# Optimization experiments

Hardware: AMD Instinct MI355X
Metric: run time of the kernel (lower is better)

Reference implementation:

```python
import jax, jax.numpy as jnp
import numpy as np

B, T, D = 2, 2048, 1024
H = 16
HD = D // H
NE = 17  # n_edge_types + 1

def setup_inputs() -> dict:
    key = jax.random.key(0)
    ks = jax.random.split(key, 6)
    x = jax.random.normal(ks[0], (B, T, D), dtype=jnp.float32)
    graph_adj = jax.random.uniform(ks[1], (B, T, T), dtype=jnp.float32)
    edge_types = jax.random.randint(ks[2], (B, T, T), 0, NE, dtype=jnp.int32)
    Wqkv = jax.random.normal(ks[3], (D, 3 * D), dtype=jnp.float32) * (D ** -0.5)
    Wproj = jax.random.normal(ks[4], (D, D), dtype=jnp.float32) * (D ** -0.5)
    adj_bias = jnp.zeros((H,), dtype=jnp.float32)
    edge_table = jax.random.normal(ks[5], (NE, H), dtype=jnp.float32) * 0.02
    return {"x": x, "graph_adj": graph_adj, "edge_types": edge_types,
            "Wqkv": Wqkv, "Wproj": Wproj, "adj_bias": adj_bias,
            "edge_table": edge_table}

def reference(x, graph_adj, edge_types, Wqkv, Wproj, adj_bias, edge_table):
    Bc, Tc, C = x.shape
    qkv = (x @ Wqkv).reshape(Bc, Tc, 3, H, HD)
    q, k, v = qkv[:, :, 0], qkv[:, :, 1], qkv[:, :, 2]  # [B,T,H,HD]
    scale = 1.0 / jnp.sqrt(jnp.asarray(HD, dtype=x.dtype))
    # scores: [B,H,T,T]
    attn = jnp.einsum('bqhd,bkhd->bhqk', q, k) * scale
    # adjacency bias per head
    attn = attn + adj_bias[None, :, None, None] * graph_adj[:, None, :, :]
    # edge-type bias: lookup [B,T,T,H] -> [B,H,T,T]
    etype_b = edge_table[edge_types]  # [B,T,T,H]
    attn = attn + jnp.transpose(etype_b, (0, 3, 1, 2))
    # causal mask (upper triangle, diag=1)
    causal = jnp.triu(jnp.ones((Tc, Tc), dtype=bool), k=1)
    attn = jnp.where(causal[None, None, :, :], jnp.asarray(-jnp.inf, dtype=attn.dtype), attn)
    attn = jax.nn.softmax(attn, axis=-1)
    out = jnp.einsum('bhqk,bkhd->bqhd', attn, v).reshape(Bc, Tc, C)
    return out @ Wproj
```

## Files before the change

### kernel.cpp

```cpp
#include <hip/hip_runtime.h>
#include <stdint.h>

#define TT 2048
#define HH 16
#define LOG2E 1.44269504089f

typedef _Float16 f16;
typedef __attribute__((ext_vector_type(8))) _Float16 f16x8;
typedef __attribute__((ext_vector_type(4))) float f32x4;
typedef unsigned short ushort_t;

__device__ __forceinline__ void gl_lds16(const void* g, void* l){
  __builtin_amdgcn_global_load_lds(
      (__attribute__((address_space(1))) void*)(void*)g,
      (__attribute__((address_space(3))) void*)l, 16, 0, 0);
}

__device__ __forceinline__ void lds_barrier(){
  __asm__ volatile("s_waitcnt lgkmcnt(0)\n\ts_barrier" ::: "memory");
}

__global__ __launch_bounds__(256) void cvt_f2h_kernel(const float4* __restrict__ in,
                                                      uint2* __restrict__ out, int n4){
  int i = blockIdx.x * 256 + threadIdx.x;
  if (i >= n4) return;
  float4 v = in[i];
  union { f16 h[4]; uint2 u; } o;
  o.h[0] = (f16)v.x; o.h[1] = (f16)v.y; o.h[2] = (f16)v.z; o.h[3] = (f16)v.w;
  out[i] = o.u;
}

__global__ __launch_bounds__(256) void transpose_cvt_kernel(const float* __restrict__ in,
                                                            f16* __restrict__ out, int R, int C){
  __shared__ float tile[64][65];
  int c0 = blockIdx.x * 64, r0 = blockIdx.y * 64;
  int t = threadIdx.x;
  int row = t >> 2, cs = (t & 3) << 4;
  const float4* src = (const float4*)(in + (size_t)(r0 + row) * C + c0 + cs);
  float4 a = src[0], b = src[1], c = src[2], d = src[3];
  float* tr = &tile[row][cs];
  tr[0]=a.x; tr[1]=a.y; tr[2]=a.z;  tr[3]=a.w;
  tr[4]=b.x; tr[5]=b.y; tr[6]=b.z;  tr[7]=b.w;
  tr[8]=c.x; tr[9]=c.y; tr[10]=c.z; tr[11]=c.w;
  tr[12]=d.x;tr[13]=d.y;tr[14]=d.z; tr[15]=d.w;
  __syncthreads();
  f16 tmp[16];
  #pragma unroll
  for (int j = 0; j < 16; ++j) tmp[j] = (f16)tile[cs + j][row];
  f16* dst = out + (size_t)(c0 + row) * R + r0 + cs;
  *(uint4*)dst = *(uint4*)&tmp[0];
  *(uint4*)(dst + 8) = *(uint4*)&tmp[8];
}

__global__ __launch_bounds__(256) void gemm_f16_kernel(const f16* __restrict__ A,
                                                       const f16* __restrict__ Bt,
                                                       void* __restrict__ Cout,
                                                       int M, int N, int K, int out_f32){
  __shared__ __align__(16) f16 As[128 * 32];
  __shared__ __align__(16) f16 Bs[128 * 32];
  int t = threadIdx.x;
  int w = t >> 6, lane = t & 63;
  int wm = (w >> 1) * 64, wn = (w & 1) * 64;
  int lrow = lane & 15, quad = lane >> 4;
  int bm = blockIdx.y, bn = blockIdx.x;

  f32x4 acc[4][4];
  for (int i = 0; i < 4; ++i)
    for (int j = 0; j < 4; ++j)
      for (int r = 0; r < 4; ++r) acc[i][j][r] = 0.f;

  const int nk = K >> 5;
  for (int kt = 0; kt < nk; ++kt){
    int k0 = kt << 5;
    __syncthreads();
    #pragma unroll
    for (int i = 0; i < 2; ++i){
      int c = (w << 7) + (i << 6) + lane;
      gl_lds16(A  + (size_t)((bm << 7) + (c >> 2)) * K + k0 + ((c & 3) << 3),
               As + ((w << 7) + (i << 6)) * 8);
      gl_lds16(Bt + (size_t)((bn << 7) + (c >> 2)) * K + k0 + ((c & 3) << 3),
               Bs + ((w << 7) + (i << 6)) * 8);
    }
    __syncthreads();
    f16x8 af[4], bfr[4];
    #pragma unroll
    for (int mi = 0; mi < 4; ++mi)
      af[mi] = *(const f16x8*)(As + (wm + mi * 16 + lrow) * 32 + quad * 8);
    #pragma unroll
    for (int ni = 0; ni < 4; ++ni)
      bfr[ni] = *(const f16x8*)(Bs + (wn + ni * 16 + lrow) * 32 + quad * 8);
    #pragma unroll
    for (int mi = 0; mi < 4; ++mi)
      #pragma unroll
      for (int ni = 0; ni < 4; ++ni)
        acc[mi][ni] = __builtin_amdgcn_mfma_f32_16x16x32_f16(af[mi], bfr[ni], acc[mi][ni], 0, 0, 0);
  }

  #pragma unroll
  for (int mi = 0; mi < 4; ++mi)
    #pragma unroll
    for (int ni = 0; ni < 4; ++ni)
      #pragma unroll
      for (int r = 0; r < 4; ++r){
        int row = (bm << 7) + wm + mi * 16 + quad * 4 + r;
        int col = (bn << 7) + wn + ni * 16 + lrow;
        float val = acc[mi][ni][r];
        if (out_f32) ((float*)Cout)[(size_t)row * N + col] = val;
        else         ((f16*)Cout)[(size_t)row * N + col] = (f16)val;
      }
}

__global__ __launch_bounds__(256, 4) void attn_kernel(const f16* __restrict__ qkv,
                                                      const float* __restrict__ gadj,
                                                      const int* __restrict__ etype,
                                                      const float* __restrict__ adj_bias,
                                                      const float* __restrict__ edge_table,
                                                      f16* __restrict__ attn_out,
                                                      f16* __restrict__ Opart,
                                                      float* __restrict__ MLpart){
  __shared__ __align__(16) f16 Ks[64 * 72];
  __shared__ __align__(16) f16 Vt[64 * 72];
  __shared__ __align__(16) f16 Ps[4][16 * 72];
  __shared__ float edge_lds[8 * 33];

  int bx = blockIdx.x;
  int h = bx & 15;
  int b = (bx >> 4) & 1;
  int j = bx >> 5;
  int qt, c0;
  if (j < 16){ qt = 16 + j; c0 = 0; }
  else { int p = (j - 16) >> 1;
         if (((j - 16) & 1) == 0){ qt = 15 - p; c0 = 0; }
         else                    { qt = 31 - p; c0 = 1; } }
  int ks = c0 << 4;
  int ke = min(qt, ks + 15);
  bool whole = (c0 == 0) && (qt <= 15);

  int t = threadIdx.x;
  int w = t >> 6, lane = t & 63;
  int lrow = lane & 15, quad = lane >> 4;

  if (t < 136){
    int cp = t / 17, e = t - cp * 17;
    edge_lds[cp * 33 + e] = edge_table[e * HH + h];
  }
  float adjb = adj_bias[h];
  int erep = (lane & 7) * 33;

  int q0 = qt * 64 + w * 16;
  const size_t qrow = ((size_t)b * TT + q0 + lrow) * 3072 + h * 64;
  f16x8 qf0 = *(const f16x8*)(qkv + qrow + quad * 8);
  f16x8 qf1 = *(const f16x8*)(qkv + qrow + 32 + quad * 8);

  f32x4 o[4];
  for (int i = 0; i < 4; ++i)
    for (int r = 0; r < 4; ++r) o[i][r] = 0.f;
  float mrun[4] = {-1e30f, -1e30f, -1e30f, -1e30f};
  float lrun[4] = {0.f, 0.f, 0.f, 0.f};

  const int keyA = t >> 3,        hdA = (t & 7) << 3;
  const int keyB = 32 + (t >> 3), hdB = hdA;
  const int sA = ((keyA >> 3) ^ (hdA >> 3)) & 7;
  const int sB = ((keyB >> 3) ^ (hdB >> 3)) & 7;
  const f16* kbase = qkv + (size_t)b * TT * 3072 + 1024 + h * 64;
  const f16* vbase = qkv + (size_t)b * TT * 3072 + 2048 + h * 64;

  for (int kt2 = ks; kt2 <= ke; ++kt2){
    lds_barrier();
    uint4 kv0 = *(const uint4*)(kbase + (size_t)(kt2 * 64 + keyA) * 3072 + hdA);
    uint4 kv1 = *(const uint4*)(kbase + (size_t)(kt2 * 64 + keyB) * 3072 + hdB);
    uint4 vv0 = *(const uint4*)(vbase + (size_t)(kt2 * 64 + keyA) * 3072 + hdA);
    uint4 vv1 = *(const uint4*)(vbase + (size_t)(kt2 * 64 + keyB) * 3072 + hdB);

    int qgb = q0 + quad * 4;
    int kgb = kt2 * 64 + lrow;
    float gv[16]; int ev[16];
    #pragma unroll
    for (int nb = 0; nb < 4; ++nb){
      size_t idx0 = ((size_t)b * TT + qgb) * TT + kgb + nb * 16;
      #pragma unroll
      for (int r = 0; r < 4; ++r){
        size_t idx = idx0 + (size_t)r * TT;
        gv[nb * 4 + r] = gadj[idx];
        ev[nb * 4 + r] = etype[idx];
      }
    }

    *(uint4*)(Ks + keyA * 72 + hdA) = kv0;
    *(uint4*)(Ks + keyB * 72 + hdB) = kv1;
    {
      union { uint4 u; f16 hh[8]; } ua, ub;
      ua.u = vv0; ub.u = vv1;
      #pragma unroll
      for (int jj = 0; jj < 8; ++jj){
        Vt[(hdA + jj) * 72 + (sA << 3) + (keyA & 7)] = ua.hh[jj];
        Vt[(hdB + jj) * 72 + (sB << 3) + (keyB & 7)] = ub.hh[jj];
      }
    }
    lds_barrier();

    f32x4 sf[4];
    #pragma unroll
    for (int nb = 0; nb < 4; ++nb){
      f32x4 s = {0.f, 0.f, 0.f, 0.f};
      f16x8 kf0 = *(const f16x8*)(Ks + (nb * 16 + lrow) * 72 + quad * 8);
      f16x8 kf1 = *(const f16x8*)(Ks + (nb * 16 + lrow) * 72 + 32 + quad * 8);
      s = __builtin_amdgcn_mfma_f32_16x16x32_f16(qf0, kf0, s, 0, 0, 0);
      s = __builtin_amdgcn_mfma_f32_16x16x32_f16(qf1, kf1, s, 0, 0, 0);
      sf[nb] = s;
    }

    float sarr[4][4];
    bool diag = (kt2 == qt);
    #pragma unroll
    for (int nb = 0; nb < 4; ++nb){
      int kg = kgb + nb * 16;
      #pragma unroll
      for (int r = 0; r < 4; ++r){
        float v;
        if (diag && kg > qgb + r) v = -1e30f;
        else v = sf[nb][r] * 0.125f + adjb * gv[nb * 4 + r] + edge_lds[erep + ev[nb * 4 + r]];
        sarr[nb][r] = v;
      }
    }

    float pv_[4][4];
    #pragma unroll
    for (int r = 0; r < 4; ++r){
      float mx = fmaxf(fmaxf(sarr[0][r], sarr[1][r]), fmaxf(sarr[2][r], sarr[3][r]));
      mx = fmaxf(mx, __shfl_xor(mx, 1));
      mx = fmaxf(mx, __shfl_xor(mx, 2));
      mx = fmaxf(mx, __shfl_xor(mx, 4));
      mx = fmaxf(mx, __shfl_xor(mx, 8));
      float mnew = fmaxf(mrun[r], mx);
      float alpha = exp2f((mrun[r] - mnew) * LOG2E);
      mrun[r] = mnew;
      float rs = 0.f;
      #pragma unroll
      for (int nb = 0; nb < 4; ++nb){
        float p = exp2f((sarr[nb][r] - mnew) * LOG2E);
        pv_[nb][r] = p; rs += p;
      }
      rs += __shfl_xor(rs, 1); rs += __shfl_xor(rs, 2);
      rs += __shfl_xor(rs, 4); rs += __shfl_xor(rs, 8);
      lrun[r] = lrun[r] * alpha + rs;
      #pragma unroll
      for (int nbh = 0; nbh < 4; ++nbh) o[nbh][r] *= alpha;
    }

    f16* Pw = &Ps[w][0];
    #pragma unroll
    for (int nb = 0; nb < 4; ++nb)
      #pragma unroll
      for (int r = 0; r < 4; ++r)
        Pw[(quad * 4 + r) * 72 + nb * 16 + lrow] = (f16)pv_[nb][r];
    __asm__ volatile("s_waitcnt lgkmcnt(0)" ::: "memory");

    #pragma unroll
    for (int cc = 0; cc < 2; ++cc){
      f16x8 pf = *(const f16x8*)(Pw + lrow * 72 + cc * 32 + quad * 8);
      #pragma unroll
      for (int nbh = 0; nbh < 4; ++nbh){
        int hd = nbh * 16 + lrow;
        int sb = (hd >> 3) & 7;
        f16x8 vf = *(const f16x8*)(Vt + hd * 72 + (((cc * 4 + quad) ^ sb) << 3));
        o[nbh] = __builtin_amdgcn_mfma_f32_16x16x32_f16(pf, vf, o[nbh], 0, 0, 0);
      }
    }
  }

  if (whole){
    float inv[4];
    #pragma unroll
    for (int r = 0; r < 4; ++r) inv[r] = 1.0f / lrun[r];
    #pragma unroll
    for (int nbh = 0; nbh < 4; ++nbh)
      #pragma unroll
      for (int r = 0; r < 4; ++r){
        int qg = q0 + quad * 4 + r;
        int col = h * 64 + nbh * 16 + lrow;
        attn_out[((size_t)b * TT + qg) * 1024 + col] = (f16)(o[nbh][r] * inv[r]);
      }
  } else {
    int slot = (((b * 16 + h) * 16) + (qt - 16)) * 2 + c0;
    f16* Ob = Opart + (size_t)slot * 4096;
    #pragma unroll
    for (int nbh = 0; nbh < 4; ++nbh)
      #pragma unroll
      for (int r = 0; r < 4; ++r)
        Ob[(w * 16 + quad * 4 + r) * 64 + nbh * 16 + lrow] = (f16)o[nbh][r];
    if (lrow == 0){
      #pragma unroll
      for (int r = 0; r < 4; ++r){
        int qq = w * 16 + quad * 4 + r;
        MLpart[(size_t)slot * 128 + qq] = mrun[r];
        MLpart[(size_t)slot * 128 + 64 + qq] = lrun[r];
      }
    }
  }
}

__global__ __launch_bounds__(256) void combine_kernel(const f16* __restrict__ Opart,
                                                      const float* __restrict__ ML,
                                                      f16* __restrict__ attn_out){
  int bx = blockIdx.x;
  int t = threadIdx.x;
  int q = t >> 2;
  int hd0 = (t & 3) << 4;
  int slot0 = bx * 2;
  float m0 = ML[(size_t)slot0 * 128 + q],       l0 = ML[(size_t)slot0 * 128 + 64 + q];
  float m1 = ML[(size_t)(slot0 + 1) * 128 + q], l1 = ML[(size_t)(slot0 + 1) * 128 + 64 + q];
  float M = fmaxf(m0, m1);
  float w0 = exp2f((m0 - M) * LOG2E), w1 = exp2f((m1 - M) * LOG2E);
  float invL = 1.0f / (l0 * w0 + l1 * w1);

  const f16* O0 = Opart + (size_t)slot0 * 4096 + q * 64 + hd0;
  const f16* O1 = O0 + 4096;
  f16x8 a0 = *(const f16x8*)O0,   a1 = *(const f16x8*)(O0 + 8);
  f16x8 b0 = *(const f16x8*)O1,   b1 = *(const f16x8*)(O1 + 8);
  f16 outv[16];
  #pragma unroll
  for (int i = 0; i < 8; ++i){
    outv[i]     = (f16)(((float)a0[i] * w0 + (float)b0[i] * w1) * invL);
    outv[i + 8] = (f16)(((float)a1[i] * w0 + (float)b1[i] * w1) * invL);
  }
  int qt = (bx & 15) + 16, h = (bx >> 4) & 15, b = bx >> 8;
  int qg = qt * 64 + q;
  f16* dst = attn_out + ((size_t)b * TT + qg) * 1024 + h * 64 + hd0;
  *(uint4*)dst = *(uint4*)&outv[0];
  *(uint4*)(dst + 8) = *(uint4*)&outv[8];
}

extern "C" void kernel_launch(void* const* d_in, const int* in_sizes, int n_in,
                              void* d_out, int out_size, void* d_ws, size_t ws_size,
                              hipStream_t stream){
  (void)in_sizes; (void)n_in; (void)out_size; (void)ws_size;
  const float* x_f32  = (const float*)d_in[0];
  const float* gadj   = (const float*)d_in[1];
  const int*   etype  = (const int*)d_in[2];
  const float* wqkv   = (const float*)d_in[3];
  const float* wproj  = (const float*)d_in[4];
  const float* adjb   = (const float*)d_in[5];
  const float* etab   = (const float*)d_in[6];

  char* ws = (char*)d_ws;
  f16*   x_f16  = (f16*)(ws);
  f16*   wqkvT  = (f16*)(ws + (8u << 20));
  f16*   wprojT = (f16*)(ws + (14u << 20));
  f16*   qkv    = (f16*)(ws + (16u << 20));
  f16*   Opart  = (f16*)(ws + (40u << 20));
  float* MLpart = (float*)(ws + (48u << 20));
  f16*   attn_o = x_f16;

  cvt_f2h_kernel<<<4096, 256, 0, stream>>>((const float4*)x_f32, (uint2*)x_f16, 1048576);
  transpose_cvt_kernel<<<dim3(48, 16), 256, 0, stream>>>(wqkv, wqkvT, 1024, 3072);
  transpose_cvt_kernel<<<dim3(16, 16), 256, 0, stream>>>(wproj, wprojT, 1024, 1024);
  gemm_f16_kernel<<<dim3(24, 32), 256, 0, stream>>>(x_f16, wqkvT, qkv, 4096, 3072, 1024, 0);
  attn_kernel<<<1536, 256, 0, stream>>>(qkv, gadj, etype, adjb, etab, attn_o, Opart, MLpart);
  combine_kernel<<<512, 256, 0, stream>>>(Opart, MLpart, attn_o);
  gemm_f16_kernel<<<dim3(8, 32), 256, 0, stream>>>(attn_o, wprojT, d_out, 4096, 1024, 1024, 1);
}
```

Measured before the change: 292.3 us.

## Fuse x conversion into QKV GEMM, prefetch bias tiles, and generalize split-K attention chunks

Result: slower. 320.2 us (+9.6%).

```diff
diff --git a/kernel.cpp b/kernel.cpp
--- a/kernel.cpp
+++ b/kernel.cpp
@@ -7,6 +7,7 @@
 
 typedef _Float16 f16;
 typedef __attribute__((ext_vector_type(8))) _Float16 f16x8;
+typedef __attribute__((ext_vector_type(2))) __fp16 fp16x2;
 typedef __attribute__((ext_vector_type(4))) float f32x4;
 typedef unsigned short ushort_t;
 
@@ -18,16 +19,6 @@
 
 __device__ __forceinline__ void lds_barrier(){
   __asm__ volatile("s_waitcnt lgkmcnt(0)\n\ts_barrier" ::: "memory");
-}
-
-__global__ __launch_bounds__(256) void cvt_f2h_kernel(const float4* __restrict__ in,
-                                                      uint2* __restrict__ out, int n4){
-  int i = blockIdx.x * 256 + threadIdx.x;
-  if (i >= n4) return;
-  float4 v = in[i];
-  union { f16 h[4]; uint2 u; } o;
-  o.h[0] = (f16)v.x; o.h[1] = (f16)v.y; o.h[2] = (f16)v.z; o.h[3] = (f16)v.w;
-  out[i] = o.u;
 }
 
 __global__ __launch_bounds__(256) void transpose_cvt_kernel(const float* __restrict__ in,
@@ -52,10 +43,82 @@
   *(uint4*)(dst + 8) = *(uint4*)&tmp[8];
 }
 
+__global__ __launch_bounds__(256) void gemm_xa_kernel(const float* __restrict__ A,
+                                                      const f16* __restrict__ Bt,
+                                                      f16* __restrict__ Cout,
+                                                      int M, int N, int K){
+  __shared__ __align__(16) f16 As[128 * 40];
+  __shared__ __align__(16) f16 Bs[128 * 32];
+  int t = threadIdx.x;
+  int w = t >> 6, lane = t & 63;
+  int wm = (w >> 1) * 64, wn = (w & 1) * 64;
+  int lrow = lane & 15, quad = lane >> 4;
+  int bm = blockIdx.y, bn = blockIdx.x;
+
+  int arow = t >> 1, acol = (t & 1) << 4;
+  const float* abase = A + (size_t)((bm << 7) + arow) * K + acol;
+
+  f32x4 acc[4][4];
+  for (int i = 0; i < 4; ++i)
+    for (int j = 0; j < 4; ++j)
+      for (int r = 0; r < 4; ++r) acc[i][j][r] = 0.f;
+
+  const int nk = K >> 5;
+  for (int kt = 0; kt < nk; ++kt){
+    int k0 = kt << 5;
+    __syncthreads();
+    {
+      const float4* ap = (const float4*)(abase + k0);
+      float4 a0 = ap[0], a1 = ap[1], a2 = ap[2], a3 = ap[3];
+      union { fp16x2 h2[8]; uint4 u[2]; } cv;
+      cv.h2[0] = __builtin_amdgcn_cvt_pkrtz(a0.x, a0.y);
+      cv.h2[1] = __builtin_amdgcn_cvt_pkrtz(a0.z, a0.w);
+      cv.h2[2] = __builtin_amdgcn_cvt_pkrtz(a1.x, a1.y);
+      cv.h2[3] = __builtin_amdgcn_cvt_pkrtz(a1.z, a1.w);
+      cv.h2[4] = __builtin_amdgcn_cvt_pkrtz(a2.x, a2.y);
+      cv.h2[5] = __builtin_amdgcn_cvt_pkrtz(a2.z, a2.w);
+      cv.h2[6] = __builtin_amdgcn_cvt_pkrtz(a3.x, a3.y);
+      cv.h2[7] = __builtin_amdgcn_cvt_pkrtz(a3.z, a3.w);
+      *(uint4*)(As + arow * 40 + acol)     = cv.u[0];
+      *(uint4*)(As + arow * 40 + acol + 8) = cv.u[1];
+    }
+    #pragma unroll
+    for (int i = 0; i < 2; ++i){
+      int c = (w << 7) + (i << 6) + lane;
+      gl_lds16(Bt + (size_t)((bn << 7) + (c >> 2)) * K + k0 + ((c & 3) << 3),
+               Bs + ((w << 7) + (i << 6)) * 8);
+    }
+    __syncthreads();
+    f16x8 af[4], bfr[4];
+    #pragma unroll
+    for (int mi = 0; mi < 4; ++mi)
+      af[mi] = *(const f16x8*)(As + (wm + mi * 16 + lrow) * 40 + quad * 8);
+    #pragma unroll
+    for (int ni = 0; ni < 4; ++ni)
+      bfr[ni] = *(const f16x8*)(Bs + (wn + ni * 16 + lrow) * 32 + quad * 8);
+    #pragma unroll
+    for (int mi = 0; mi < 4; ++mi)
+      #pragma unroll
+      for (int ni = 0; ni < 4; ++ni)
+        acc[mi][ni] = __builtin_amdgcn_mfma_f32_16x16x32_f16(af[mi], bfr[ni], acc[mi][ni], 0, 0, 0);
+  }
+
+  #pragma unroll
+  for (int mi = 0; mi < 4; ++mi)
+    #pragma unroll
+    for (int ni = 0; ni < 4; ++ni)
+      #pragma unroll
+      for (int r = 0; r < 4; ++r){
+        int row = (bm << 7) + wm + mi * 16 + quad * 4 + r;
+        int col = (bn << 7) + wn + ni * 16 + lrow;
+        Cout[(size_t)row * N + col] = (f16)acc[mi][ni][r];
+      }
+}
+
 __global__ __launch_bounds__(256) void gemm_f16_kernel(const f16* __restrict__ A,
                                                        const f16* __restrict__ Bt,
-                                                       void* __restrict__ Cout,
-                                                       int M, int N, int K, int out_f32){
+                                                       float* __restrict__ Cout,
+                                                       int M, int N, int K){
   __shared__ __align__(16) f16 As[128 * 32];
   __shared__ __align__(16) f16 Bs[128 * 32];
   int t = threadIdx.x;
@@ -104,9 +167,7 @@
       for (int r = 0; r < 4; ++r){
         int row = (bm << 7) + wm + mi * 16 + quad * 4 + r;
         int col = (bn << 7) + wn + ni * 16 + lrow;
-        float val = acc[mi][ni][r];
-        if (out_f32) ((float*)Cout)[(size_t)row * N + col] = val;
-        else         ((f16*)Cout)[(size_t)row * N + col] = (f16)val;
+        Cout[(size_t)row * N + col] = acc[mi][ni][r];
       }
 }
 
@@ -117,24 +178,22 @@
                                                       const float* __restrict__ edge_table,
                                                       f16* __restrict__ attn_out,
                                                       f16* __restrict__ Opart,
-                                                      float* __restrict__ MLpart){
+                                                      float* __restrict__ MLpart,
+                                                      int CH, int NQT, int MAXCH){
   __shared__ __align__(16) f16 Ks[64 * 72];
   __shared__ __align__(16) f16 Vt[64 * 72];
   __shared__ __align__(16) f16 Ps[4][16 * 72];
   __shared__ float edge_lds[8 * 33];
 
-  int bx = blockIdx.x;
-  int h = bx & 15;
-  int b = (bx >> 4) & 1;
-  int j = bx >> 5;
-  int qt, c0;
-  if (j < 16){ qt = 16 + j; c0 = 0; }
-  else { int p = (j - 16) >> 1;
-         if (((j - 16) & 1) == 0){ qt = 15 - p; c0 = 0; }
-         else                    { qt = 31 - p; c0 = 1; } }
-  int ks = c0 << 4;
-  int ke = min(qt, ks + 15);
-  bool whole = (c0 == 0) && (qt <= 15);
+  int bh = blockIdx.x;
+  int h = bh & 15;
+  int b = bh >> 4;
+  int qt = 31 - (int)blockIdx.y;
+  int c0 = blockIdx.z;
+  int ks = c0 * CH;
+  if (ks > qt) return;
+  int ke = min(qt, ks + CH - 1);
+  bool whole = (qt < CH);
 
   int t = threadIdx.x;
   int w = t >> 6, lane = t & 63;
@@ -148,9 +207,12 @@
   int erep = (lane & 7) * 33;
 
   int q0 = qt * 64 + w * 16;
+  int qgb = q0 + quad * 4;
   const size_t qrow = ((size_t)b * TT + q0 + lrow) * 3072 + h * 64;
   f16x8 qf0 = *(const f16x8*)(qkv + qrow + quad * 8);
   f16x8 qf1 = *(const f16x8*)(qkv + qrow + 32 + quad * 8);
+  #pragma unroll
+  for (int i = 0; i < 8; ++i){ qf0[i] *= (f16)0.125f; qf1[i] *= (f16)0.125f; }
 
   f32x4 o[4];
   for (int i = 0; i < 4; ++i)
@@ -165,26 +227,28 @@
   const f16* kbase = qkv + (size_t)b * TT * 3072 + 1024 + h * 64;
   const f16* vbase = qkv + (size_t)b * TT * 3072 + 2048 + h * 64;
 
+  float gv[16]; int ev[16];
+  auto load_bias = [&](int kt){
+    int kg0 = kt * 64 + lrow;
+    #pragma unroll
+    for (int nb = 0; nb < 4; ++nb){
+      size_t idx0 = ((size_t)b * TT + qgb) * TT + kg0 + nb * 16;
+      #pragma unroll
+      for (int r = 0; r < 4; ++r){
+        size_t idx = idx0 + (size_t)r * TT;
+        gv[nb * 4 + r] = gadj[idx];
+        ev[nb * 4 + r] = etype[idx];
+      }
+    }
+  };
+  load_bias(ks);
+
   for (int kt2 = ks; kt2 <= ke; ++kt2){
     lds_barrier();
     uint4 kv0 = *(const uint4*)(kbase + (size_t)(kt2 * 64 + keyA) * 3072 + hdA);
     uint4 kv1 = *(const uint4*)(kbase + (size_t)(kt2 * 64 + keyB) * 3072 + hdB);
     uint4 vv0 = *(const uint4*)(vbase + (size_t)(kt2 * 64 + keyA) * 3072 + hdA);
     uint4 vv1 = *(const uint4*)(vbase + (size_t)(kt2 * 64 + keyB) * 3072 + hdB);
-
-    int qgb = q0 + quad * 4;
-    int kgb = kt2 * 64 + lrow;
-    float gv[16]; int ev[16];
-    #pragma unroll
-    for (int nb = 0; nb < 4; ++nb){
-      size_t idx0 = ((size_t)b * TT + qgb) * TT + kgb + nb * 16;
-      #pragma unroll
-      for (int r = 0; r < 4; ++r){
-        size_t idx = idx0 + (size_t)r * TT;
-        gv[nb * 4 + r] = gadj[idx];
-        ev[nb * 4 + r] = etype[idx];
-      }
-    }
 
     *(uint4*)(Ks + keyA * 72 + hdA) = kv0;
     *(uint4*)(Ks + keyB * 72 + hdB) = kv1;
@@ -214,15 +278,17 @@
     bool diag = (kt2 == qt);
     #pragma unroll
     for (int nb = 0; nb < 4; ++nb){
-      int kg = kgb + nb * 16;
+      int kg = kt2 * 64 + lrow + nb * 16;
       #pragma unroll
       for (int r = 0; r < 4; ++r){
         float v;
         if (diag && kg > qgb + r) v = -1e30f;
-        else v = sf[nb][r] * 0.125f + adjb * gv[nb * 4 + r] + edge_lds[erep + ev[nb * 4 + r]];
+        else v = sf[nb][r] + fmaf(adjb, gv[nb * 4 + r], edge_lds[erep + ev[nb * 4 + r]]);
         sarr[nb][r] = v;
       }
     }
+
+    load_bias(kt2 < ke ? kt2 + 1 : ke);
 
     float pv_[4][4];
     #pragma unroll
@@ -282,7 +348,7 @@
         attn_out[((size_t)b * TT + qg) * 1024 + col] = (f16)(o[nbh][r] * inv[r]);
       }
   } else {
-    int slot = (((b * 16 + h) * 16) + (qt - 16)) * 2 + c0;
+    int slot = (bh * NQT + (qt - CH)) * MAXCH + c0;
     f16* Ob = Opart + (size_t)slot * 4096;
     #pragma unroll
     for (int nbh = 0; nbh < 4; ++nbh)
@@ -302,29 +368,43 @@
 
 __global__ __launch_bounds__(256) void combine_kernel(const f16* __restrict__ Opart,
                                                       const float* __restrict__ ML,
-                                                      f16* __restrict__ attn_out){
-  int bx = blockIdx.x;
+                                                      f16* __restrict__ attn_out,
+                                                      int CH, int NQT, int MAXCH){
+  int bh = blockIdx.x, qy = blockIdx.y;
+  int qt = CH + qy;
+  int h = bh & 15, b = bh >> 4;
+  int nch = (qt + CH) / CH;
   int t = threadIdx.x;
   int q = t >> 2;
   int hd0 = (t & 3) << 4;
-  int slot0 = bx * 2;
-  float m0 = ML[(size_t)slot0 * 128 + q],       l0 = ML[(size_t)slot0 * 128 + 64 + q];
-  float m1 = ML[(size_t)(slot0 + 1) * 128 + q], l1 = ML[(size_t)(slot0 + 1) * 128 + 64 + q];
-  float M = fmaxf(m0, m1);
-  float w0 = exp2f((m0 - M) * LOG2E), w1 = exp2f((m1 - M) * LOG2E);
-  float invL = 1.0f / (l0 * w0 + l1 * w1);
-
-  const f16* O0 = Opart + (size_t)slot0 * 4096 + q * 64 + hd0;
-  const f16* O1 = O0 + 4096;
-  f16x8 a0 = *(const f16x8*)O0,   a1 = *(const f16x8*)(O0 + 8);
-  f16x8 b0 = *(const f16x8*)O1,   b1 = *(const f16x8*)(O1 + 8);
+  int slot0 = (bh * NQT + qy) * MAXCH;
+
+  float m[4], l[4], wgt[4];
+  float M = -1e30f;
+  for (int c = 0; c < nch; ++c){
+    m[c] = ML[(size_t)(slot0 + c) * 128 + q];
+    l[c] = ML[(size_t)(slot0 + c) * 128 + 64 + q];
+    M = fmaxf(M, m[c]);
+  }
+  float L = 0.f;
+  for (int c = 0; c < nch; ++c){ wgt[c] = exp2f((m[c] - M) * LOG2E); L += l[c] * wgt[c]; }
+  float invL = 1.0f / L;
+
+  float acc[16];
+  #pragma unroll
+  for (int i = 0; i < 16; ++i) acc[i] = 0.f;
+  for (int c = 0; c < nch; ++c){
+    const f16* O = Opart + (size_t)(slot0 + c) * 4096 + q * 64 + hd0;
+    f16x8 a0 = *(const f16x8*)O, a1 = *(const f16x8*)(O + 8);
+    #pragma unroll
+    for (int i = 0; i < 8; ++i){
+      acc[i]     += wgt[c] * (float)a0[i];
+      acc[i + 8] += wgt[c] * (float)a1[i];
+    }
+  }
   f16 outv[16];
   #pragma unroll
-  for (int i = 0; i < 8; ++i){
-    outv[i]     = (f16)(((float)a0[i] * w0 + (float)b0[i] * w1) * invL);
-    outv[i + 8] = (f16)(((float)a1[i] * w0 + (float)b1[i] * w1) * invL);
-  }
-  int qt = (bx & 15) + 16, h = (bx >> 4) & 15, b = bx >> 8;
+  for (int i = 0; i < 16; ++i) outv[i] = (f16)(acc[i] * invL);
   int qg = qt * 64 + q;
   f16* dst = attn_out + ((size_t)b * TT + qg) * 1024 + h * 64 + hd0;
   *(uint4*)dst = *(uint4*)&outv[0];
@@ -334,7 +414,7 @@
 extern "C" void kernel_launch(void* const* d_in, const int* in_sizes, int n_in,
                               void* d_out, int out_size, void* d_ws, size_t ws_size,
                               hipStream_t stream){
-  (void)in_sizes; (void)n_in; (void)out_size; (void)ws_size;
+  (void)in_sizes; (void)n_in; (void)out_size;
   const float* x_f32  = (const float*)d_in[0];
   const float* gadj   = (const float*)d_in[1];
   const int*   etype  = (const int*)d_in[2];
@@ -343,20 +423,24 @@
   const float* adjb   = (const float*)d_in[5];
   const float* etab   = (const float*)d_in[6];
 
+  const int CH    = (ws_size >= 62390272ull) ? 8 : 16;
+  const int NQT   = 32 - CH;
+  const int MAXCH = (CH == 8) ? 4 : 2;
+
   char* ws = (char*)d_ws;
-  f16*   x_f16  = (f16*)(ws);
-  f16*   wqkvT  = (f16*)(ws + (8u << 20));
-  f16*   wprojT = (f16*)(ws + (14u << 20));
-  f16*   qkv    = (f16*)(ws + (16u << 20));
-  f16*   Opart  = (f16*)(ws + (40u << 20));
-  float* MLpart = (float*)(ws + (48u << 20));
-  f16*   attn_o = x_f16;
-
-  cvt_f2h_kernel<<<4096, 256, 0, stream>>>((const float4*)x_f32, (uint2*)x_f16, 1048576);
+  f16*   qkv    = (f16*)(ws);
+  f16*   attn_o = (f16*)(ws + 25165824);
+  f16*   wprojT = (f16*)(ws + 33554432);
+  f16*   wqkvT  = (f16*)(ws + 35651584);
+  f16*   Opart  = (f16*)(ws + 35651584);
+  size_t opart_bytes = (size_t)32 * NQT * MAXCH * 4096 * 2;
+  float* MLpart = (float*)(ws + 35651584 + opart_bytes);
+
   transpose_cvt_kernel<<<dim3(48, 16), 256, 0, stream>>>(wqkv, wqkvT, 1024, 3072);
   transpose_cvt_kernel<<<dim3(16, 16), 256, 0, stream>>>(wproj, wprojT, 1024, 1024);
-  gemm_f16_kernel<<<dim3(24, 32), 256, 0, stream>>>(x_f16, wqkvT, qkv, 4096, 3072, 1024, 0);
-  attn_kernel<<<1536, 256, 0, stream>>>(qkv, gadj, etype, adjb, etab, attn_o, Opart, MLpart);
-  combine_kernel<<<512, 256, 0, stream>>>(Opart, MLpart, attn_o);
-  gemm_f16_kernel<<<dim3(8, 32), 256, 0, stream>>>(attn_o, wprojT, d_out, 4096, 1024, 1024, 1);
-}
+  gemm_xa_kernel<<<dim3(24, 32), 256, 0, stream>>>(x_f32, wqkvT, qkv, 4096, 3072, 1024);
+  attn_kernel<<<dim3(32, 32, MAXCH), 256, 0, stream>>>(qkv, gadj, etype, adjb, etab,
+                                                       attn_o, Opart, MLpart, CH, NQT, MAXCH);
+  combine_kernel<<<dim3(32, NQT), 256, 0, stream>>>(Opart, MLpart, attn_o, CH, NQT, MAXCH);
+  gemm_f16_kernel<<<dim3(8, 32), 256, 0, stream>>>(attn_o, wprojT, (float*)d_out, 4096, 1024, 1024);
+}
```
